# Performance work log

Measured on AMD Instinct MI355X. Metric: run time of the kernel, lower is better.

The kernel has to match this reference:

```python
import jax, jax.numpy as jnp
import numpy as np

B, S, M = 128, 4096, 20
LOG_2PI = float(np.log(2.0 * np.pi))


def setup_inputs() -> dict:
    key = jax.random.key(0)
    k1, k2, k3, k4, k5 = jax.random.split(key, 5)
    xs = jax.random.normal(k1, (B, S, 5), dtype=jnp.float32)
    logits_pred = jax.random.normal(k2, (B, S, M), dtype=jnp.float32)
    mus_pred = jax.random.normal(k3, (B, S, M, 2), dtype=jnp.float32)
    # sigmas are Cholesky entries (l00, l10, l11); diagonal must be positive.
    sigmas_pred = jax.random.uniform(k4, (B, S, M, 3), dtype=jnp.float32) + 0.1
    pen_pred = jax.random.uniform(k5, (B, S, 3), dtype=jnp.float32)
    return {"xs": xs, "logits_pred": logits_pred, "mus_pred": mus_pred,
            "sigmas_pred": sigmas_pred, "pen_pred": pen_pred}


def reference(xs, logits_pred, mus_pred, sigmas_pred, pen_pred):
    # split stroke-5 format: (dx_abs, dy_abs) + 3 pen states
    position_true = xs[..., :2]          # [B,S,2]
    pen_true = xs[..., 2:]               # [B,S,3]

    # relative positions: roll by 1 along seq, first step prev = (0,0)
    position_prev = jnp.concatenate(
        [jnp.zeros_like(position_true[:, :1]), position_true[:, :-1]], axis=1)
    rel = position_true - position_prev  # [B,S,2]

    # closed-form 2D Gaussian log-density with lower-tri Cholesky
    # scale_tril entries (tril_indices(2,2) order): l00, l10, l11
    l00 = sigmas_pred[..., 0]            # [B,S,M]
    l10 = sigmas_pred[..., 1]
    l11 = sigmas_pred[..., 2]
    d = rel[:, :, None, :] - mus_pred    # [B,S,M,2]
    z0 = d[..., 0] / l00
    z1 = (d[..., 1] - l10 * z0) / l11
    comp_logp = (-0.5 * (z0 * z0 + z1 * z1)
                 - LOG_2PI - jnp.log(l00) - jnp.log(l11))  # [B,S,M]

    # mixture log-prob via logsumexp over components
    mix_logp = jax.nn.logsumexp(
        jax.nn.log_softmax(logits_pred, axis=-1) + comp_logp, axis=-1)  # [B,S]
    position_loss = -jnp.sum(mix_logp)

    # pen loss: faithful to source -> CrossEntropyLoss(input=pen_true, target=pen_pred)
    # (soft-target CE, mean reduction over B*S rows)
    logp = jax.nn.log_softmax(pen_true.reshape(-1, 3), axis=-1)
    pen_loss = jnp.mean(-jnp.sum(pen_pred.reshape(-1, 3) * logp, axis=-1))

    return position_loss + pen_loss
```

## Files before the change

### kernel.cpp

```cpp
#include <hip/hip_runtime.h>
#include <math.h>

#define BB 128
#define SS 4096
#define MM 20
#define NPOS (BB * SS)
#define BLOCK 256
#define NBLOCKS (NPOS / BLOCK)

__device__ __forceinline__ float fast_rcp(float x) { return __builtin_amdgcn_rcpf(x); }

__global__ __launch_bounds__(BLOCK, 1) void sketch_main(
    const float* __restrict__ xs,
    const float* __restrict__ logits,
    const float* __restrict__ mus,
    const float* __restrict__ sigmas,
    const float* __restrict__ pen_pred,
    float* __restrict__ partials)
{
    const float LOG_2PI = 1.8378770664093453f;
    const int p = blockIdx.x * BLOCK + threadIdx.x;
    const int s = p & (SS - 1);

    const float4* sp = (const float4*)(sigmas + (size_t)p * 60);
    const float4* mp = (const float4*)(mus    + (size_t)p * 40);
    const float4* lp = (const float4*)(logits + (size_t)p * 20);

    float4 S[15], M[10], L[5];
#pragma unroll
    for (int i = 0; i < 15; ++i) S[i] = sp[i];
#pragma unroll
    for (int i = 0; i < 10; ++i) M[i] = mp[i];
#pragma unroll
    for (int i = 0; i < 5;  ++i) L[i] = lp[i];

    const float* xp = xs + (size_t)p * 5;
    float px = xp[0], py = xp[1];
    float pt0 = xp[2], pt1 = xp[3], pt2 = xp[4];
    float qx = 0.0f, qy = 0.0f;
    if (s != 0) { qx = xp[-5]; qy = xp[-4]; }
    const float* pp = pen_pred + (size_t)p * 3;
    float pp0 = pp[0], pp1 = pp[1], pp2 = pp[2];

    const float rx = px - qx, ry = py - qy;

    float a[20];
    float sel = 0.0f;
#pragma unroll
    for (int g = 0; g < 5; ++g) {
        float sv[12] = { S[3*g].x,   S[3*g].y,   S[3*g].z,   S[3*g].w,
                         S[3*g+1].x, S[3*g+1].y, S[3*g+1].z, S[3*g+1].w,
                         S[3*g+2].x, S[3*g+2].y, S[3*g+2].z, S[3*g+2].w };
        float mv[8]  = { M[2*g].x,   M[2*g].y,   M[2*g].z,   M[2*g].w,
                         M[2*g+1].x, M[2*g+1].y, M[2*g+1].z, M[2*g+1].w };
        float lv[4]  = { L[g].x, L[g].y, L[g].z, L[g].w };
#pragma unroll
        for (int c = 0; c < 4; ++c) {
            float l00 = sv[3*c], l10 = sv[3*c+1], l11 = sv[3*c+2];
            float z0 = (rx - mv[2*c]) * fast_rcp(l00);
            float z1 = ((ry - mv[2*c+1]) - l10 * z0) * fast_rcp(l11);
            a[4*g+c] = lv[c] - 0.5f * (z0*z0 + z1*z1) - LOG_2PI - __logf(l00 * l11);
            sel += __expf(lv[c]);
        }
    }

    float mx = a[0];
#pragma unroll
    for (int c = 1; c < MM; ++c) mx = fmaxf(mx, a[c]);
    float se = 0.0f;
#pragma unroll
    for (int c = 0; c < MM; ++c) se += __expf(a[c] - mx);
    float mix_logp = (mx + __logf(se)) - __logf(sel);

    float pm = fmaxf(pt0, fmaxf(pt1, pt2));
    float lse3 = pm + __logf(__expf(pt0 - pm) + __expf(pt1 - pm) + __expf(pt2 - pm));
    float pen = -(pp0 * (pt0 - lse3) + pp1 * (pt1 - lse3) + pp2 * (pt2 - lse3));

    float val = -mix_logp + pen * (1.0f / (float)NPOS);

#pragma unroll
    for (int off = 32; off > 0; off >>= 1) val += __shfl_down(val, off, 64);
    __shared__ float red[BLOCK / 64];
    int lane = threadIdx.x & 63, wid = threadIdx.x >> 6;
    if (lane == 0) red[wid] = val;
    __syncthreads();
    if (threadIdx.x == 0)
        partials[blockIdx.x] = red[0] + red[1] + red[2] + red[3];
}

__global__ __launch_bounds__(256) void sketch_reduce(
    const float* __restrict__ partials, float* __restrict__ out)
{
    float v = 0.0f;
    for (int i = threadIdx.x; i < NBLOCKS; i += 256) v += partials[i];
#pragma unroll
    for (int off = 32; off > 0; off >>= 1) v += __shfl_down(v, off, 64);
    __shared__ float red[4];
    int lane = threadIdx.x & 63, wid = threadIdx.x >> 6;
    if (lane == 0) red[wid] = v;
    __syncthreads();
    if (threadIdx.x == 0)
        out[0] = red[0] + red[1] + red[2] + red[3];
}

extern "C" void kernel_launch(void* const* d_in, const int* in_sizes, int n_in,
                              void* d_out, int out_size, void* d_ws, size_t ws_size,
                              hipStream_t stream) {
    const float* xs       = (const float*)d_in[0];
    const float* logits   = (const float*)d_in[1];
    const float* mus      = (const float*)d_in[2];
    const float* sigmas   = (const float*)d_in[3];
    const float* pen_pred = (const float*)d_in[4];
    float* out = (float*)d_out;
    float* partials = (float*)d_ws;

    sketch_main<<<NBLOCKS, BLOCK, 0, stream>>>(xs, logits, mus, sigmas, pen_pred, partials);
    sketch_reduce<<<1, 256, 0, stream>>>(partials, out);
}
```

Baseline: 277.9 us.

## Stage mixture params through padded LDS for coalesced global loads

Each thread previously loaded its own contiguous 240/160/80-byte slice of sigmas, mus and logits, so a wavefront's loads were strided. Now the block cooperatively loads a contiguous chunk with lane-consecutive float4 reads, transposes it into padded shared-memory rows, and each thread reads its position's parameters from LDS. Block size drops to 128 positions to fit the roughly 63 KB of LDS. The cost is an extra LDS write/read pass plus a barrier, and the larger LDS footprint limits how many blocks can be resident per CU.

```diff
diff --git a/kernel.cpp b/kernel.cpp
--- a/kernel.cpp
+++ b/kernel.cpp
@@ -5,12 +5,13 @@
 #define SS 4096
 #define MM 20
 #define NPOS (BB * SS)
-#define BLOCK 256
-#define NBLOCKS (NPOS / BLOCK)
+#define POSB 128
+#define THREADS 128
+#define NBLOCKS (NPOS / POSB)
 
 __device__ __forceinline__ float fast_rcp(float x) { return __builtin_amdgcn_rcpf(x); }
 
-__global__ __launch_bounds__(BLOCK, 1) void sketch_main(
+__global__ __launch_bounds__(THREADS, 1) void sketch_main(
     const float* __restrict__ xs,
     const float* __restrict__ logits,
     const float* __restrict__ mus,
@@ -19,20 +20,26 @@
     float* __restrict__ partials)
 {
     const float LOG_2PI = 1.8378770664093453f;
-    const int p = blockIdx.x * BLOCK + threadIdx.x;
-    const int s = p & (SS - 1);
+    __shared__ float sig_l[POSB * 61];
+    __shared__ float mu_l [POSB * 41];
+    __shared__ float lg_l [POSB * 21];
 
-    const float4* sp = (const float4*)(sigmas + (size_t)p * 60);
-    const float4* mp = (const float4*)(mus    + (size_t)p * 40);
-    const float4* lp = (const float4*)(logits + (size_t)p * 20);
+    const int t  = threadIdx.x;
+    const int pb = blockIdx.x * POSB;
+    const int p  = pb + t;
+    const int s  = p & (SS - 1);
 
-    float4 S[15], M[10], L[5];
+    const float4* gs = (const float4*)(sigmas + (size_t)pb * 60);
+    const float4* gm = (const float4*)(mus    + (size_t)pb * 40);
+    const float4* gl = (const float4*)(logits + (size_t)pb * 20);
+
+    float4 vs[15], vm[10], vl[5];
 #pragma unroll
-    for (int i = 0; i < 15; ++i) S[i] = sp[i];
+    for (int i = 0; i < 15; ++i) vs[i] = gs[t + THREADS * i];
 #pragma unroll
-    for (int i = 0; i < 10; ++i) M[i] = mp[i];
+    for (int i = 0; i < 10; ++i) vm[i] = gm[t + THREADS * i];
 #pragma unroll
-    for (int i = 0; i < 5;  ++i) L[i] = lp[i];
+    for (int i = 0; i < 5;  ++i) vl[i] = gl[t + THREADS * i];
 
     const float* xp = xs + (size_t)p * 5;
     float px = xp[0], py = xp[1];
@@ -42,26 +49,50 @@
     const float* pp = pen_pred + (size_t)p * 3;
     float pp0 = pp[0], pp1 = pp[1], pp2 = pp[2];
 
+    {
+        int q = t / 15, r = t % 15;
+#pragma unroll
+        for (int i = 0; i < 15; ++i) {
+            float* d = &sig_l[q * 61 + r * 4];
+            d[0] = vs[i].x; d[1] = vs[i].y; d[2] = vs[i].z; d[3] = vs[i].w;
+            q += 8; r += 8; if (r >= 15) { r -= 15; q += 1; }
+        }
+    }
+    {
+        int q = t / 10, r = t % 10;
+#pragma unroll
+        for (int i = 0; i < 10; ++i) {
+            float* d = &mu_l[q * 41 + r * 4];
+            d[0] = vm[i].x; d[1] = vm[i].y; d[2] = vm[i].z; d[3] = vm[i].w;
+            q += 12; r += 8; if (r >= 10) { r -= 10; q += 1; }
+        }
+    }
+    {
+        int q = t / 5, r = t % 5;
+#pragma unroll
+        for (int i = 0; i < 5; ++i) {
+            float* d = &lg_l[q * 21 + r * 4];
+            d[0] = vl[i].x; d[1] = vl[i].y; d[2] = vl[i].z; d[3] = vl[i].w;
+            q += 25; r += 3; if (r >= 5) { r -= 5; q += 1; }
+        }
+    }
+    __syncthreads();
+
     const float rx = px - qx, ry = py - qy;
+    const float* sl = &sig_l[t * 61];
+    const float* ml = &mu_l [t * 41];
+    const float* ll = &lg_l [t * 21];
 
     float a[20];
     float sel = 0.0f;
 #pragma unroll
-    for (int g = 0; g < 5; ++g) {
-        float sv[12] = { S[3*g].x,   S[3*g].y,   S[3*g].z,   S[3*g].w,
-                         S[3*g+1].x, S[3*g+1].y, S[3*g+1].z, S[3*g+1].w,
-                         S[3*g+2].x, S[3*g+2].y, S[3*g+2].z, S[3*g+2].w };
-        float mv[8]  = { M[2*g].x,   M[2*g].y,   M[2*g].z,   M[2*g].w,
-                         M[2*g+1].x, M[2*g+1].y, M[2*g+1].z, M[2*g+1].w };
-        float lv[4]  = { L[g].x, L[g].y, L[g].z, L[g].w };
-#pragma unroll
-        for (int c = 0; c < 4; ++c) {
-            float l00 = sv[3*c], l10 = sv[3*c+1], l11 = sv[3*c+2];
-            float z0 = (rx - mv[2*c]) * fast_rcp(l00);
-            float z1 = ((ry - mv[2*c+1]) - l10 * z0) * fast_rcp(l11);
-            a[4*g+c] = lv[c] - 0.5f * (z0*z0 + z1*z1) - LOG_2PI - __logf(l00 * l11);
-            sel += __expf(lv[c]);
-        }
+    for (int c = 0; c < MM; ++c) {
+        float l00 = sl[3*c], l10 = sl[3*c+1], l11 = sl[3*c+2];
+        float z0 = (rx - ml[2*c]) * fast_rcp(l00);
+        float z1 = ((ry - ml[2*c+1]) - l10 * z0) * fast_rcp(l11);
+        float lg = ll[c];
+        a[c] = lg - 0.5f * (z0*z0 + z1*z1) - LOG_2PI - __logf(l00 * l11);
+        sel += __expf(lg);
     }
 
     float mx = a[0];
@@ -80,12 +111,12 @@
 
 #pragma unroll
     for (int off = 32; off > 0; off >>= 1) val += __shfl_down(val, off, 64);
-    __shared__ float red[BLOCK / 64];
-    int lane = threadIdx.x & 63, wid = threadIdx.x >> 6;
+    __shared__ float red[THREADS / 64];
+    int lane = t & 63, wid = t >> 6;
     if (lane == 0) red[wid] = val;
     __syncthreads();
-    if (threadIdx.x == 0)
-        partials[blockIdx.x] = red[0] + red[1] + red[2] + red[3];
+    if (t == 0)
+        partials[blockIdx.x] = red[0] + red[1];
 }
 
 __global__ __launch_bounds__(256) void sketch_reduce(
@@ -114,6 +145,6 @@
     float* out = (float*)d_out;
     float* partials = (float*)d_ws;
 
-    sketch_main<<<NBLOCKS, BLOCK, 0, stream>>>(xs, logits, mus, sigmas, pen_pred, partials);
+    sketch_main<<<NBLOCKS, THREADS, 0, stream>>>(xs, logits, mus, sigmas, pen_pred, partials);
     sketch_reduce<<<1, 256, 0, stream>>>(partials, out);
 }
```

After: 285.7 us. +2.8%, slower.

## Double-buffer per-thread component loads and raise occupancy hint

Applied to the files above, without the earlier changes.

Replaces the single up-front load of all 30 float4 values per thread with scalar loads in four chunks of five components, ping-ponging between two register buffers so a chunk's loads are issued while the previous chunk is computed. It also changes launch bounds from 1 to 4 to push register use down and allow more resident waves. The cost targeted is register pressure and low occupancy that limit memory latency hiding. The scalar float loads may not be merged back into wide vector loads, since chunk offsets like 15*k break 16-byte alignment, so the number of load instructions could rise.

```diff
diff --git a/kernel.cpp b/kernel.cpp
--- a/kernel.cpp
+++ b/kernel.cpp
@@ -10,7 +10,7 @@
 
 __device__ __forceinline__ float fast_rcp(float x) { return __builtin_amdgcn_rcpf(x); }
 
-__global__ __launch_bounds__(BLOCK, 1) void sketch_main(
+__global__ __launch_bounds__(BLOCK, 4) void sketch_main(
     const float* __restrict__ xs,
     const float* __restrict__ logits,
     const float* __restrict__ mus,
@@ -22,17 +22,9 @@
     const int p = blockIdx.x * BLOCK + threadIdx.x;
     const int s = p & (SS - 1);
 
-    const float4* sp = (const float4*)(sigmas + (size_t)p * 60);
-    const float4* mp = (const float4*)(mus    + (size_t)p * 40);
-    const float4* lp = (const float4*)(logits + (size_t)p * 20);
-
-    float4 S[15], M[10], L[5];
-#pragma unroll
-    for (int i = 0; i < 15; ++i) S[i] = sp[i];
-#pragma unroll
-    for (int i = 0; i < 10; ++i) M[i] = mp[i];
-#pragma unroll
-    for (int i = 0; i < 5;  ++i) L[i] = lp[i];
+    const float* sp = sigmas + (size_t)p * 60;
+    const float* mp = mus    + (size_t)p * 40;
+    const float* lp = logits + (size_t)p * 20;
 
     const float* xp = xs + (size_t)p * 5;
     float px = xp[0], py = xp[1];
@@ -41,28 +33,41 @@
     if (s != 0) { qx = xp[-5]; qy = xp[-4]; }
     const float* pp = pen_pred + (size_t)p * 3;
     float pp0 = pp[0], pp1 = pp[1], pp2 = pp[2];
-
     const float rx = px - qx, ry = py - qy;
 
     float a[20];
     float sel = 0.0f;
-#pragma unroll
-    for (int g = 0; g < 5; ++g) {
-        float sv[12] = { S[3*g].x,   S[3*g].y,   S[3*g].z,   S[3*g].w,
-                         S[3*g+1].x, S[3*g+1].y, S[3*g+1].z, S[3*g+1].w,
-                         S[3*g+2].x, S[3*g+2].y, S[3*g+2].z, S[3*g+2].w };
-        float mv[8]  = { M[2*g].x,   M[2*g].y,   M[2*g].z,   M[2*g].w,
-                         M[2*g+1].x, M[2*g+1].y, M[2*g+1].z, M[2*g+1].w };
-        float lv[4]  = { L[g].x, L[g].y, L[g].z, L[g].w };
-#pragma unroll
-        for (int c = 0; c < 4; ++c) {
-            float l00 = sv[3*c], l10 = sv[3*c+1], l11 = sv[3*c+2];
-            float z0 = (rx - mv[2*c]) * fast_rcp(l00);
-            float z1 = ((ry - mv[2*c+1]) - l10 * z0) * fast_rcp(l11);
-            a[4*g+c] = lv[c] - 0.5f * (z0*z0 + z1*z1) - LOG_2PI - __logf(l00 * l11);
-            sel += __expf(lv[c]);
-        }
-    }
+
+    float sA[15], mA[10], lA[5];
+    float sB[15], mB[10], lB[5];
+
+#define LOADC(k, Sv, Mv, Lv) do {                                   \
+    _Pragma("unroll") for (int j = 0; j < 15; ++j) Sv[j] = sp[15*(k)+j]; \
+    _Pragma("unroll") for (int j = 0; j < 10; ++j) Mv[j] = mp[10*(k)+j]; \
+    _Pragma("unroll") for (int j = 0; j <  5; ++j) Lv[j] = lp[ 5*(k)+j]; \
+  } while (0)
+
+#define COMPC(k, Sv, Mv, Lv) do {                                   \
+    _Pragma("unroll") for (int c = 0; c < 5; ++c) {                 \
+        float l00 = Sv[3*c], l10 = Sv[3*c+1], l11 = Sv[3*c+2];      \
+        float z0 = (rx - Mv[2*c]) * fast_rcp(l00);                  \
+        float z1 = ((ry - Mv[2*c+1]) - l10 * z0) * fast_rcp(l11);   \
+        float lg = Lv[c];                                           \
+        a[5*(k)+c] = lg - 0.5f*(z0*z0 + z1*z1) - LOG_2PI - __logf(l00 * l11); \
+        sel += __expf(lg);      \
+    } } while (0)
+
+    LOADC(0, sA, mA, lA);
+    LOADC(1, sB, mB, lB);
+    COMPC(0, sA, mA, lA);
+    LOADC(2, sA, mA, lA);
+    COMPC(1, sB, mB, lB);
+    LOADC(3, sB, mB, lB);
+    COMPC(2, sA, mA, lA);
+    COMPC(3, sB, mB, lB);
+
+#undef LOADC
+#undef COMPC
 
     float mx = a[0];
 #pragma unroll
```

Measured after the change: 309.5 us. 11.4% more time.
